# Kernel tuning notes

Hardware: AMD Instinct MI355X
Metric: run time of the kernel (lower is better)

## Reference

```python
import jax, jax.numpy as jnp
import numpy as np
import math

B, N, EMB, DK = 4, 4096, 512, 64

def setup_inputs() -> dict:
    key = jax.random.key(0)
    ks = jax.random.split(key, 4)
    E = jax.random.normal(ks[0], (B, N, EMB), dtype=jnp.float32)
    mask = jnp.tril(jnp.ones((1, N, N), dtype=jnp.int32))  # causal mask, 0 = masked
    s = 1.0 / math.sqrt(EMB)
    wq_kernel = jax.random.normal(ks[1], (EMB, DK), dtype=jnp.float32) * s
    wk_kernel = jax.random.normal(ks[2], (EMB, DK), dtype=jnp.float32) * s
    wv_kernel = jax.random.normal(ks[3], (EMB, EMB), dtype=jnp.float32) * s
    return {
        "E": E, "mask": mask,
        "wq_kernel": wq_kernel, "wq_bias": jnp.zeros((DK,), jnp.float32),
        "wk_kernel": wk_kernel, "wk_bias": jnp.zeros((DK,), jnp.float32),
        "wv_kernel": wv_kernel, "wv_bias": jnp.zeros((EMB,), jnp.float32),
    }

def reference(E, mask, wq_kernel, wq_bias, wk_kernel, wk_bias, wv_kernel, wv_bias):
    # Dense projections (flax Dense: x @ kernel + bias)
    Q = jnp.einsum('bne,ed->bnd', E, wq_kernel) + wq_bias   # [B,N,DK]
    K = jnp.einsum('bne,ed->bnd', E, wk_kernel) + wk_bias   # [B,N,DK]
    V = jnp.einsum('bne,ed->bnd', E, wv_kernel) + wv_bias   # [B,N,EMB]
    scores = jnp.einsum('bqd,bkd->bqk', Q, K) / math.sqrt(Q.shape[-1])  # [B,N,N]
    scores = jnp.where(mask == 0, float('-inf'), scores)
    attention = jax.nn.softmax(scores, axis=-1)
    return jnp.einsum('bqk,bke->bqe', attention, V)  # [B,N,EMB]
```

## Files before the change

kernel.cpp:

```cpp
#include <hip/hip_runtime.h>
#include <hip/hip_bf16.h>

typedef float f32x4 __attribute__((ext_vector_type(4)));
typedef __bf16 bf16x8 __attribute__((ext_vector_type(8)));
typedef __bf16 bf16x4 __attribute__((ext_vector_type(4)));
typedef unsigned short ushort4v __attribute__((ext_vector_type(4)));
typedef unsigned short ushort8v __attribute__((ext_vector_type(8)));

#define MFMA16(a, b, c) __builtin_amdgcn_mfma_f32_16x16x32_bf16((a), (b), (c), 0, 0, 0)

__device__ __forceinline__ unsigned short f2bf(float f) {
    union { float f; unsigned int u; } v; v.f = f;
    unsigned int r = (v.u + 0x7fffu + ((v.u >> 16) & 1u)) >> 16;
    return (unsigned short)r;
}
__device__ __forceinline__ int imin(int a, int b) { return a < b ? a : b; }
__device__ __forceinline__ float fexp2(float x) {
    float r; asm("v_exp_f32 %0, %1" : "=v"(r) : "v"(x)); return r;
}

__device__ __forceinline__ void ldsbar() {
    asm volatile("s_waitcnt lgkmcnt(0)" ::: "memory");
    __builtin_amdgcn_s_barrier();
}

__global__ __launch_bounds__(256) void prep_w(const float* __restrict__ wq,
                                              const float* __restrict__ wk,
                                              const float* __restrict__ wv,
                                              unsigned short* __restrict__ Fqk,
                                              unsigned short* __restrict__ Fv)
{
    const int t = blockIdx.x * 256 + threadIdx.x;
    if (t < 8192) {
        const int lane = t & 63, kt = (t >> 6) & 15, ct = t >> 10;
        const int g = lane >> 4, li = lane & 15;
        const int c = ct * 16 + li;
        const int k0 = kt * 32 + g * 8;
        ushort8v u;
        if (c < 64) {
#pragma unroll
            for (int j = 0; j < 8; ++j) u[j] = f2bf(wq[(size_t)(k0 + j) * 64 + c]);
        } else {
#pragma unroll
            for (int j = 0; j < 8; ++j) u[j] = f2bf(wk[(size_t)(k0 + j) * 64 + (c - 64)]);
        }
        *(ushort8v*)&Fqk[(size_t)t * 8] = u;
    } else {
        const int t2 = t - 8192;
        const int lane = t2 & 63, kt = (t2 >> 6) & 15, ct = t2 >> 10;
        const int g = lane >> 4, li = lane & 15;
        const int c = ct * 16 + li;
        const int k0 = kt * 32 + g * 8;
        ushort8v u;
#pragma unroll
        for (int j = 0; j < 8; ++j) u[j] = f2bf(wv[(size_t)(k0 + j) * 512 + c]);
        *(ushort8v*)&Fv[(size_t)t2 * 8] = u;
    }
}

__global__ __launch_bounds__(512) void proj_kernel(const float* __restrict__ E,
        const unsigned short* __restrict__ Fqk, const unsigned short* __restrict__ Fv,
        const float* __restrict__ bq, const float* __restrict__ bk, const float* __restrict__ bv,
        unsigned short* __restrict__ Qb, unsigned short* __restrict__ Kb,
        unsigned short* __restrict__ Vt)
{
    __shared__ __align__(16) unsigned short Al[2][128][40];

    const int tid = threadIdx.x;
    const int w = tid >> 6, l = tid & 63, g = l >> 4, li = l & 15;
    const int wm = w >> 2, wn = w & 3;
    const int bx = blockIdx.x, by = blockIdx.y;
    const int row0 = bx * 128;
    const int arow = tid >> 2, ak = (tid & 3) * 8;
    const float* ebase = &E[(size_t)(row0 + arow) * 512 + ak];
    const float QSCALE = 0.125f * 1.4426950408889634f;

#define LOAD_E(kt, dst)                                                          \
    {                                                                            \
        const float* ep = ebase + (kt) * 32;                                     \
        f32x4 v0 = *(const f32x4*)ep;                                            \
        f32x4 v1 = *(const f32x4*)(ep + 4);                                      \
        _Pragma("unroll")                                                        \
        for (int j = 0; j < 4; ++j) { dst[j] = f2bf(v0[j]); dst[4 + j] = f2bf(v1[j]); } \
    }

    if (by == 0) {
        f32x4 acc[4][2];
#pragma unroll
        for (int mb = 0; mb < 4; ++mb)
#pragma unroll
            for (int nb = 0; nb < 2; ++nb) acc[mb][nb] = (f32x4)0.0f;

        bf16x8 bw[2], bwn[2];
        {
            ushort8v e0; LOAD_E(0, e0);
            *(ushort8v*)&Al[0][arow][ak] = e0;
#pragma unroll
            for (int nb = 0; nb < 2; ++nb) {
                const int ct = wn * 2 + nb;
                bw[nb] = *(const bf16x8*)&Fqk[((size_t)(ct * 16 + 0) * 64 + l) * 8];
            }
        }
        ldsbar();

        for (int kt = 0; kt < 16; ++kt) {
            const int buf = kt & 1;
            ushort8v en;
            if (kt < 15) LOAD_E(kt + 1, en);
            const int ktn = imin(kt + 1, 15);
#pragma unroll
            for (int nb = 0; nb < 2; ++nb) {
                const int ct = wn * 2 + nb;
                bwn[nb] = *(const bf16x8*)&Fqk[((size_t)(ct * 16 + ktn) * 64 + l) * 8];
            }
            bf16x8 af[4];
#pragma unroll
            for (int mb = 0; mb < 4; ++mb)
                af[mb] = *(const bf16x8*)&Al[buf][wm * 64 + mb * 16 + li][8 * g];
#pragma unroll
            for (int mb = 0; mb < 4; ++mb)
#pragma unroll
                for (int nb = 0; nb < 2; ++nb) acc[mb][nb] = MFMA16(af[mb], bw[nb], acc[mb][nb]);
            if (kt < 15) *(ushort8v*)&Al[buf ^ 1][arow][ak] = en;
            ldsbar();
            bw[0] = bwn[0]; bw[1] = bwn[1];
        }

#pragma unroll
        for (int mb = 0; mb < 4; ++mb) {
#pragma unroll
            for (int nb = 0; nb < 2; ++nb) {
                const int coll = wn * 32 + nb * 16 + li;
                const int grow0 = row0 + wm * 64 + mb * 16 + 4 * g;
                if (coll < 64) {
                    const float bb = bq[coll];
#pragma unroll
                    for (int r = 0; r < 4; ++r)
                        Qb[(size_t)(grow0 + r) * 64 + coll] = f2bf((acc[mb][nb][r] + bb) * QSCALE);
                } else {
                    const float bb = bk[coll - 64];
#pragma unroll
                    for (int r = 0; r < 4; ++r)
                        Kb[(size_t)(grow0 + r) * 64 + (coll - 64)] = f2bf(acc[mb][nb][r] + bb);
                }
            }
        }
    } else {
        const int vy = by - 1;
        f32x4 acc[4][4];
#pragma unroll
        for (int mb = 0; mb < 4; ++mb)
#pragma unroll
            for (int nb = 0; nb < 4; ++nb) acc[mb][nb] = (f32x4)0.0f;

        bf16x8 bw[4], bwn[4];
        {
            ushort8v e0; LOAD_E(0, e0);
            *(ushort8v*)&Al[0][arow][ak] = e0;
#pragma unroll
            for (int nb = 0; nb < 4; ++nb) {
                const int ct = vy * 16 + wn * 4 + nb;
                bw[nb] = *(const bf16x8*)&Fv[((size_t)(ct * 16 + 0) * 64 + l) * 8];
            }
        }
        ldsbar();

        for (int kt = 0; kt < 16; ++kt) {
            const int buf = kt & 1;
            ushort8v en;
            if (kt < 15) LOAD_E(kt + 1, en);
            const int ktn = imin(kt + 1, 15);
#pragma unroll
            for (int nb = 0; nb < 4; ++nb) {
                const int ct = vy * 16 + wn * 4 + nb;
                bwn[nb] = *(const bf16x8*)&Fv[((size_t)(ct * 16 + ktn) * 64 + l) * 8];
            }
            bf16x8 af[4];
#pragma unroll
            for (int mb = 0; mb < 4; ++mb)
                af[mb] = *(const bf16x8*)&Al[buf][wm * 64 + mb * 16 + li][8 * g];
#pragma unroll
            for (int mb = 0; mb < 4; ++mb)
#pragma unroll
                for (int nb = 0; nb < 4; ++nb) acc[mb][nb] = MFMA16(af[mb], bw[nb], acc[mb][nb]);
            if (kt < 15) *(ushort8v*)&Al[buf ^ 1][arow][ak] = en;
            ldsbar();
#pragma unroll
            for (int nb = 0; nb < 4; ++nb) bw[nb] = bwn[nb];
        }

#pragma unroll
        for (int mb = 0; mb < 4; ++mb) {
#pragma unroll
            for (int nb = 0; nb < 4; ++nb) {
                const int col = vy * 256 + wn * 64 + nb * 16 + li;
                const int grow0 = row0 + wm * 64 + mb * 16 + 4 * g;
                const float bb = bv[col];
                ushort4v u;
#pragma unroll
                for (int r = 0; r < 4; ++r) u[r] = f2bf(acc[mb][nb][r] + bb);
                const int bbatch = grow0 >> 12, n = grow0 & 4095;
                *(ushort4v*)(Vt + ((size_t)bbatch * 512 + col) * 4096 + n) = u;
            }
        }
    }
#undef LOAD_E
}

__global__ __launch_bounds__(256) void attn_kernel(const unsigned short* __restrict__ Qb,
                                                   const unsigned short* __restrict__ Kb,
                                                   const unsigned short* __restrict__ Vt,
                                                   float* __restrict__ out)
{
    __shared__ __align__(16) unsigned short Kl[2][64][64];
    __shared__ __align__(16) unsigned short Pl[2][64][76];
    __shared__ float scl[2][64];
    __shared__ __align__(16) float dfl[2][4];
    __shared__ float lsum_l[64];

    const int tid = threadIdx.x;
    const int w = tid >> 6, lane = tid & 63, g = lane >> 4, li = lane & 15;
    const int bid = blockIdx.x;
    const int x = bid >> 4, b = (bid >> 2) & 3, ch = bid & 3;
    const int k4 = x >> 4, r4 = x & 15;
    const int qt = (k4 == 0) ? r4 : (k4 == 1) ? (63 - r4) : (k4 == 2) ? (16 + r4) : (47 - r4);
    const int q0 = qt * 64;
    const int niter = qt + 1;
    const int qrow = 16 * w + li;

    const unsigned short* qptr = Qb + ((size_t)(b * 4096 + q0 + qrow)) * 64 + 8 * g;
    const bf16x8 QA0 = *(const bf16x8*)qptr;
    const bf16x8 QA1 = *(const bf16x8*)(qptr + 32);

    float m_r = -INFINITY, l_r = 0.0f;
    f32x4 Of[4][2];
#pragma unroll
    for (int qb = 0; qb < 4; ++qb) { Of[qb][0] = (f32x4)0.0f; Of[qb][1] = (f32x4)0.0f; }

    const int cglob = ch * 128 + w * 32 + li;
    const unsigned short* vbase = Vt + ((size_t)(b * 512 + cglob)) * 4096 + 8 * g;

    const int krow = tid >> 3, kch = tid & 7;
    const unsigned short* kgb = Kb + ((size_t)(b * 4096 + krow)) * 64 + kch * 8;
    const int kslot = (kch ^ (krow & 7)) * 8;

    {
        ushort8v v0 = *(const ushort8v*)(kgb);
        ushort8v v1 = *(const ushort8v*)(kgb + 32 * 64);
        *(ushort8v*)&Kl[0][krow][kslot] = v0;
        *(ushort8v*)&Kl[0][krow + 32][kslot] = v1;
    }
    ldsbar();

    for (int j = 0; j < niter; ++j) {
        const int buf = j & 1;
        const size_t kv0 = (size_t)j * 64;
        const bool havenext = (j + 1 < niter);

        const size_t kvn = (size_t)imin(j + 1, qt) * 4096;
        ushort8v kn0 = *(const ushort8v*)(kgb + kvn);
        ushort8v kn1 = *(const ushort8v*)(kgb + kvn + 32 * 64);

        bf16x8 VA[2][2];
#pragma unroll
        for (int cf = 0; cf < 2; ++cf)
#pragma unroll
            for (int ks = 0; ks < 2; ++ks)
                VA[cf][ks] = *(const bf16x8*)(vbase + (size_t)cf * 16 * 4096 + kv0 + ks * 32);

        f32x4 S[4];
        {
            const unsigned short(*Kt)[64] = Kl[buf];
            __builtin_amdgcn_s_setprio(1);
#pragma unroll
            for (int cb = 0; cb < 4; ++cb) {
                const int row = cb * 16 + li;
                bf16x8 K0 = *(const bf16x8*)&Kt[row][((g) ^ (row & 7)) * 8];
                bf16x8 K1 = *(const bf16x8*)&Kt[row][((4 + g) ^ (row & 7)) * 8];
                f32x4 s = (f32x4)0.0f;
                s = MFMA16(K0, QA0, s);
                s = MFMA16(K1, QA1, s);
                S[cb] = s;
            }
            __builtin_amdgcn_s_setprio(0);
        }
        if (j == qt) {
#pragma unroll
            for (int cb = 0; cb < 4; ++cb)
#pragma unroll
                for (int rr = 0; rr < 4; ++rr)
                    if (cb * 16 + 4 * g + rr > qrow) S[cb][rr] = -1e30f;
        }
        f32x4 m4 = S[0];
#pragma unroll
        for (int cb = 1; cb < 4; ++cb)
#pragma unroll
            for (int rr = 0; rr < 4; ++rr) m4[rr] = fmaxf(m4[rr], S[cb][rr]);
        const float pmL = fmaxf(fmaxf(m4[0], m4[1]), fmaxf(m4[2], m4[3]));

        const bool nore = __all(pmL - m_r <= 8.0f);
        float sc = 1.0f;
        if (!nore) {
            float pm = fmaxf(pmL, __shfl_xor(pmL, 16));
            pm = fmaxf(pm, __shfl_xor(pm, 32));
            const float mn = fmaxf(m_r, pm);
            sc = fexp2(m_r - mn);
            m_r = mn;
        }
        float rs = 0.0f;
#pragma unroll
        for (int cb = 0; cb < 4; ++cb) {
            bf16x4 pk;
#pragma unroll
            for (int rr = 0; rr < 4; ++rr) {
                const float pv = fexp2(S[cb][rr] - m_r);
                rs += pv;
                pk[rr] = (__bf16)pv;
            }
            *(bf16x4*)&Pl[buf][qrow][cb * 16 + 4 * g] = pk;
        }
        l_r = l_r * sc + rs;
        if (g == 0) scl[buf][qrow] = sc;
        if (lane == 0) dfl[buf][w] = nore ? 1.0f : 0.0f;

        if (havenext) {
            *(ushort8v*)&Kl[buf ^ 1][krow][kslot] = kn0;
            *(ushort8v*)&Kl[buf ^ 1][krow + 32][kslot] = kn1;
        }
        ldsbar();

        f32x4 df = *(const f32x4*)&dfl[buf][0];
        const bool allskip = (df[0] + df[1] + df[2] + df[3]) == 4.0f;
        __builtin_amdgcn_s_setprio(1);
#pragma unroll
        for (int qb = 0; qb < 4; ++qb) {
            bf16x8 PA0 = *(const bf16x8*)&Pl[buf][qb * 16 + li][8 * g];
            bf16x8 PA1 = *(const bf16x8*)&Pl[buf][qb * 16 + li][32 + 8 * g];
            if (!allskip) {
                f32x4 scv = *(const f32x4*)&scl[buf][qb * 16 + 4 * g];
#pragma unroll
                for (int cf = 0; cf < 2; ++cf)
#pragma unroll
                    for (int rr = 0; rr < 4; ++rr) Of[qb][cf][rr] *= scv[rr];
            }
#pragma unroll
            for (int cf = 0; cf < 2; ++cf) {
                f32x4 o = Of[qb][cf];
                o = MFMA16(PA0, VA[cf][0], o);
                o = MFMA16(PA1, VA[cf][1], o);
                Of[qb][cf] = o;
            }
        }
        __builtin_amdgcn_s_setprio(0);
    }

    l_r += __shfl_xor(l_r, 16);
    l_r += __shfl_xor(l_r, 32);
    if (g == 0) lsum_l[qrow] = l_r;
    ldsbar();

    float* obase = out + (size_t)(b * 4096 + q0 + 4 * g) * 512 + cglob;
#pragma unroll
    for (int qb = 0; qb < 4; ++qb) {
        f32x4 lv = *(const f32x4*)&lsum_l[qb * 16 + 4 * g];
#pragma unroll
        for (int cf = 0; cf < 2; ++cf)
#pragma unroll
            for (int rr = 0; rr < 4; ++rr)
                obase[(size_t)(qb * 16 + rr) * 512 + cf * 16] = Of[qb][cf][rr] / lv[rr];
    }
}

extern "C" void kernel_launch(void* const* d_in, const int* in_sizes, int n_in,
                              void* d_out, int out_size, void* d_ws, size_t ws_size,
                              hipStream_t stream)
{
    (void)in_sizes; (void)n_in; (void)out_size; (void)ws_size;
    const float* E  = (const float*)d_in[0];
    const float* wq = (const float*)d_in[2];
    const float* bq = (const float*)d_in[3];
    const float* wk = (const float*)d_in[4];
    const float* bk = (const float*)d_in[5];
    const float* wv = (const float*)d_in[6];
    const float* bv = (const float*)d_in[7];

    const size_t qk_elems = (size_t)4 * 4096 * 64;
    const size_t vt_elems = (size_t)4 * 512 * 4096;

    unsigned short* Qb  = (unsigned short*)d_ws;
    unsigned short* Kb  = Qb + qk_elems;
    unsigned short* Vt  = Kb + qk_elems;
    unsigned short* Fqk = Vt + vt_elems;
    unsigned short* Fv  = Fqk + (size_t)8192 * 8;
    float* out = (float*)d_out;

    prep_w<<<dim3(160), 256, 0, stream>>>(wq, wk, wv, Fqk, Fv);
    proj_kernel<<<dim3(128, 3), 512, 0, stream>>>(E, Fqk, Fv, bq, bk, bv, Qb, Kb, Vt);
    attn_kernel<<<dim3(1024), 256, 0, stream>>>(Qb, Kb, Vt, out);
}
```

Before: 116.0 us.

## Balance causal attention work by splitting heavy query tiles and merging partials

Causal attention work is rebalanced by pairing query tile hi=63-t with lo=t. One block handles the first 33 key tiles of hi. The other handles the remaining key tiles of hi plus all of lo, so every block does roughly 33 iterations. Partial outputs with running max and sum are written to a workspace buffer and combined by a new merge kernel. The aim is to remove the tail imbalance of the triangular workload, at the cost of an extra kernel launch and extra fp32 global traffic for the partials, and only when the workspace is large enough.

```diff
diff --git a/kernel.cpp b/kernel.cpp
--- a/kernel.cpp
+++ b/kernel.cpp
@@ -207,57 +207,30 @@
 #undef LOAD_E
 }
 
-__global__ __launch_bounds__(256) void attn_kernel(const unsigned short* __restrict__ Qb,
-                                                   const unsigned short* __restrict__ Kb,
-                                                   const unsigned short* __restrict__ Vt,
-                                                   float* __restrict__ out)
-{
-    __shared__ __align__(16) unsigned short Kl[2][64][64];
-    __shared__ __align__(16) unsigned short Pl[2][64][76];
-    __shared__ float scl[2][64];
-    __shared__ __align__(16) float dfl[2][4];
-    __shared__ float lsum_l[64];
-
-    const int tid = threadIdx.x;
-    const int w = tid >> 6, lane = tid & 63, g = lane >> 4, li = lane & 15;
-    const int bid = blockIdx.x;
-    const int x = bid >> 4, b = (bid >> 2) & 3, ch = bid & 3;
-    const int k4 = x >> 4, r4 = x & 15;
-    const int qt = (k4 == 0) ? r4 : (k4 == 1) ? (63 - r4) : (k4 == 2) ? (16 + r4) : (47 - r4);
-    const int q0 = qt * 64;
-    const int niter = qt + 1;
-    const int qrow = 16 * w + li;
-
-    const unsigned short* qptr = Qb + ((size_t)(b * 4096 + q0 + qrow)) * 64 + 8 * g;
-    const bf16x8 QA0 = *(const bf16x8*)qptr;
-    const bf16x8 QA1 = *(const bf16x8*)(qptr + 32);
-
-    float m_r = -INFINITY, l_r = 0.0f;
-    f32x4 Of[4][2];
-#pragma unroll
-    for (int qb = 0; qb < 4; ++qb) { Of[qb][0] = (f32x4)0.0f; Of[qb][1] = (f32x4)0.0f; }
-
-    const int cglob = ch * 128 + w * 32 + li;
-    const unsigned short* vbase = Vt + ((size_t)(b * 512 + cglob)) * 4096 + 8 * g;
-
-    const int krow = tid >> 3, kch = tid & 7;
-    const unsigned short* kgb = Kb + ((size_t)(b * 4096 + krow)) * 64 + kch * 8;
-    const int kslot = (kch ^ (krow & 7)) * 8;
-
+__device__ __forceinline__ void attn_segment(int kt0, int cnt, int qcur,
+        const unsigned short* __restrict__ kgb, int krow, int kslot,
+        const unsigned short* __restrict__ vbase,
+        bf16x8 QA0, bf16x8 QA1,
+        int w, int lane, int g, int li, int qrow,
+        float& m_r, float& l_r, f32x4 (&Of)[4][2],
+        unsigned short (*Kl)[64][64], unsigned short (*Pl)[64][76],
+        float (*scl)[64], float (*dfl)[4])
+{
     {
-        ushort8v v0 = *(const ushort8v*)(kgb);
-        ushort8v v1 = *(const ushort8v*)(kgb + 32 * 64);
+        ushort8v v0 = *(const ushort8v*)(kgb + (size_t)kt0 * 4096);
+        ushort8v v1 = *(const ushort8v*)(kgb + (size_t)kt0 * 4096 + 32 * 64);
         *(ushort8v*)&Kl[0][krow][kslot] = v0;
         *(ushort8v*)&Kl[0][krow + 32][kslot] = v1;
     }
     ldsbar();
 
-    for (int j = 0; j < niter; ++j) {
+    for (int j = 0; j < cnt; ++j) {
         const int buf = j & 1;
-        const size_t kv0 = (size_t)j * 64;
-        const bool havenext = (j + 1 < niter);
-
-        const size_t kvn = (size_t)imin(j + 1, qt) * 4096;
+        const int kt = kt0 + j;
+        const size_t kv0 = (size_t)kt * 64;
+        const bool havenext = (j + 1 < cnt);
+
+        const size_t kvn = (size_t)(kt0 + imin(j + 1, cnt - 1)) * 4096;
         ushort8v kn0 = *(const ushort8v*)(kgb + kvn);
         ushort8v kn1 = *(const ushort8v*)(kgb + kvn + 32 * 64);
 
@@ -284,7 +257,7 @@
             }
             __builtin_amdgcn_s_setprio(0);
         }
-        if (j == qt) {
+        if (kt == qcur) {
 #pragma unroll
             for (int cb = 0; cb < 4; ++cb)
 #pragma unroll
@@ -353,6 +326,163 @@
         }
         __builtin_amdgcn_s_setprio(0);
     }
+}
+
+__global__ __launch_bounds__(256) void attn_split(const unsigned short* __restrict__ Qb,
+                                                  const unsigned short* __restrict__ Kb,
+                                                  const unsigned short* __restrict__ Vt,
+                                                  float* __restrict__ Pa,
+                                                  float* __restrict__ out)
+{
+    __shared__ __align__(16) unsigned short Kl[2][64][64];
+    __shared__ __align__(16) unsigned short Pl[2][64][76];
+    __shared__ float scl[2][64];
+    __shared__ __align__(16) float dfl[2][4];
+    __shared__ float lsum_l[64];
+
+    const int tid = threadIdx.x;
+    const int w = tid >> 6, lane = tid & 63, g = lane >> 4, li = lane & 15;
+    const int bid = blockIdx.x;
+    const int half = bid & 1;
+    const int rest = bid >> 1;
+    const int t = rest >> 4, b = (rest >> 2) & 3, ch = rest & 3;
+    const int hi = 63 - t, lo = t;
+    const int qrow = 16 * w + li;
+
+    const int cglob = ch * 128 + w * 32 + li;
+    const unsigned short* vbase = Vt + ((size_t)(b * 512 + cglob)) * 4096 + 8 * g;
+    const int krow = tid >> 3, kch = tid & 7;
+    const unsigned short* kgb = Kb + ((size_t)(b * 4096 + krow)) * 64 + kch * 8;
+    const int kslot = (kch ^ (krow & 7)) * 8;
+
+    float m_r = -INFINITY, l_r = 0.0f;
+    f32x4 Of[4][2];
+#pragma unroll
+    for (int qb = 0; qb < 4; ++qb) { Of[qb][0] = (f32x4)0.0f; Of[qb][1] = (f32x4)0.0f; }
+
+    float* rec = Pa + ((size_t)(half * 512 + rest)) * 8320;
+
+    if (half == 0) {
+        const unsigned short* qptr = Qb + ((size_t)(b * 4096 + hi * 64 + qrow)) * 64 + 8 * g;
+        attn_segment(0, 33, hi, kgb, krow, kslot, vbase,
+                     *(const bf16x8*)qptr, *(const bf16x8*)(qptr + 32),
+                     w, lane, g, li, qrow, m_r, l_r, Of, Kl, Pl, scl, dfl);
+        float lred = l_r + __shfl_xor(l_r, 16);
+        lred += __shfl_xor(lred, 32);
+#pragma unroll
+        for (int qb = 0; qb < 4; ++qb)
+#pragma unroll
+            for (int cf = 0; cf < 2; ++cf)
+#pragma unroll
+                for (int rr = 0; rr < 4; ++rr)
+                    rec[(size_t)(qb * 16 + 4 * g + rr) * 128 + (w * 32 + li) + cf * 16] = Of[qb][cf][rr];
+        if (g == 0) { rec[8192 + qrow] = m_r; rec[8256 + qrow] = lred; }
+    } else {
+        const int cnt1 = 31 - t;
+        if (cnt1 > 0) {
+            const unsigned short* qptr = Qb + ((size_t)(b * 4096 + hi * 64 + qrow)) * 64 + 8 * g;
+            attn_segment(33, cnt1, hi, kgb, krow, kslot, vbase,
+                         *(const bf16x8*)qptr, *(const bf16x8*)(qptr + 32),
+                         w, lane, g, li, qrow, m_r, l_r, Of, Kl, Pl, scl, dfl);
+        }
+        float lred = l_r + __shfl_xor(l_r, 16);
+        lred += __shfl_xor(lred, 32);
+#pragma unroll
+        for (int qb = 0; qb < 4; ++qb)
+#pragma unroll
+            for (int cf = 0; cf < 2; ++cf)
+#pragma unroll
+                for (int rr = 0; rr < 4; ++rr)
+                    rec[(size_t)(qb * 16 + 4 * g + rr) * 128 + (w * 32 + li) + cf * 16] = Of[qb][cf][rr];
+        if (g == 0) { rec[8192 + qrow] = m_r; rec[8256 + qrow] = lred; }
+        m_r = -INFINITY; l_r = 0.0f;
+#pragma unroll
+        for (int qb = 0; qb < 4; ++qb) { Of[qb][0] = (f32x4)0.0f; Of[qb][1] = (f32x4)0.0f; }
+        {
+            const unsigned short* qptr = Qb + ((size_t)(b * 4096 + lo * 64 + qrow)) * 64 + 8 * g;
+            attn_segment(0, t + 1, lo, kgb, krow, kslot, vbase,
+                         *(const bf16x8*)qptr, *(const bf16x8*)(qptr + 32),
+                         w, lane, g, li, qrow, m_r, l_r, Of, Kl, Pl, scl, dfl);
+        }
+        l_r += __shfl_xor(l_r, 16);
+        l_r += __shfl_xor(l_r, 32);
+        if (g == 0) lsum_l[qrow] = l_r;
+        ldsbar();
+        float* obase = out + (size_t)(b * 4096 + lo * 64 + 4 * g) * 512 + cglob;
+#pragma unroll
+        for (int qb = 0; qb < 4; ++qb) {
+            f32x4 lv = *(const f32x4*)&lsum_l[qb * 16 + 4 * g];
+#pragma unroll
+            for (int cf = 0; cf < 2; ++cf)
+#pragma unroll
+                for (int rr = 0; rr < 4; ++rr)
+                    obase[(size_t)(qb * 16 + rr) * 512 + cf * 16] = Of[qb][cf][rr] / lv[rr];
+        }
+    }
+}
+
+__global__ __launch_bounds__(256) void merge_kernel(const float* __restrict__ Pa,
+                                                    float* __restrict__ out)
+{
+    const int pid = blockIdx.x;
+    const int t = pid >> 4, b = (pid >> 2) & 3, ch = pid & 3;
+    const int hi = 63 - t;
+    const float* A = Pa + (size_t)pid * 8320;
+    const float* B = Pa + (size_t)(512 + pid) * 8320;
+    const int tid = threadIdx.x;
+#pragma unroll
+    for (int k = 0; k < 8; ++k) {
+        const int vidx = k * 256 + tid;
+        const int row = vidx >> 5;
+        const int col4 = (vidx & 31) * 4;
+        const float ma = A[8192 + row], mb = B[8192 + row];
+        const float mF = fmaxf(ma, mb);
+        const float aA = fexp2(ma - mF), aB = fexp2(mb - mF);
+        const float l = aA * A[8256 + row] + aB * B[8256 + row];
+        f32x4 oa = *(const f32x4*)&A[(size_t)row * 128 + col4];
+        f32x4 ob = *(const f32x4*)&B[(size_t)row * 128 + col4];
+        f32x4 r;
+#pragma unroll
+        for (int j = 0; j < 4; ++j) r[j] = (aA * oa[j] + aB * ob[j]) / l;
+        *(f32x4*)&out[((size_t)(b * 4096 + hi * 64 + row)) * 512 + ch * 128 + col4] = r;
+    }
+}
+
+__global__ __launch_bounds__(256) void attn_kernel(const unsigned short* __restrict__ Qb,
+                                                   const unsigned short* __restrict__ Kb,
+                                                   const unsigned short* __restrict__ Vt,
+                                                   float* __restrict__ out)
+{
+    __shared__ __align__(16) unsigned short Kl[2][64][64];
+    __shared__ __align__(16) unsigned short Pl[2][64][76];
+    __shared__ float scl[2][64];
+    __shared__ __align__(16) float dfl[2][4];
+    __shared__ float lsum_l[64];
+
+    const int tid = threadIdx.x;
+    const int w = tid >> 6, lane = tid & 63, g = lane >> 4, li = lane & 15;
+    const int bid = blockIdx.x;
+    const int x = bid >> 4, b = (bid >> 2) & 3, ch = bid & 3;
+    const int k4 = x >> 4, r4 = x & 15;
+    const int qt = (k4 == 0) ? r4 : (k4 == 1) ? (63 - r4) : (k4 == 2) ? (16 + r4) : (47 - r4);
+    const int q0 = qt * 64;
+    const int qrow = 16 * w + li;
+
+    const int cglob = ch * 128 + w * 32 + li;
+    const unsigned short* vbase = Vt + ((size_t)(b * 512 + cglob)) * 4096 + 8 * g;
+    const int krow = tid >> 3, kch = tid & 7;
+    const unsigned short* kgb = Kb + ((size_t)(b * 4096 + krow)) * 64 + kch * 8;
+    const int kslot = (kch ^ (krow & 7)) * 8;
+
+    float m_r = -INFINITY, l_r = 0.0f;
+    f32x4 Of[4][2];
+#pragma unroll
+    for (int qb = 0; qb < 4; ++qb) { Of[qb][0] = (f32x4)0.0f; Of[qb][1] = (f32x4)0.0f; }
+
+    const unsigned short* qptr = Qb + ((size_t)(b * 4096 + q0 + qrow)) * 64 + 8 * g;
+    attn_segment(0, qt + 1, qt, kgb, krow, kslot, vbase,
+                 *(const bf16x8*)qptr, *(const bf16x8*)(qptr + 32),
+                 w, lane, g, li, qrow, m_r, l_r, Of, Kl, Pl, scl, dfl);
 
     l_r += __shfl_xor(l_r, 16);
     l_r += __shfl_xor(l_r, 32);
@@ -375,7 +505,7 @@
                               void* d_out, int out_size, void* d_ws, size_t ws_size,
                               hipStream_t stream)
 {
-    (void)in_sizes; (void)n_in; (void)out_size; (void)ws_size;
+    (void)in_sizes; (void)n_in; (void)out_size;
     const float* E  = (const float*)d_in[0];
     const float* wq = (const float*)d_in[2];
     const float* bq = (const float*)d_in[3];
@@ -392,9 +522,18 @@
     unsigned short* Vt  = Kb + qk_elems;
     unsigned short* Fqk = Vt + vt_elems;
     unsigned short* Fv  = Fqk + (size_t)8192 * 8;
+    float* Pa = (float*)(Fv + (size_t)32768 * 8);
     float* out = (float*)d_out;
+
+    const size_t base_bytes = (2 * qk_elems + vt_elems + (size_t)8192 * 8 + (size_t)32768 * 8) * 2;
+    const size_t need_split = base_bytes + (size_t)1024 * 8320 * 4;
 
     prep_w<<<dim3(160), 256, 0, stream>>>(wq, wk, wv, Fqk, Fv);
     proj_kernel<<<dim3(128, 3), 512, 0, stream>>>(E, Fqk, Fv, bq, bk, bv, Qb, Kb, Vt);
-    attn_kernel<<<dim3(1024), 256, 0, stream>>>(Qb, Kb, Vt, out);
-}
+    if (ws_size >= need_split) {
+        attn_split<<<dim3(1024), 256, 0, stream>>>(Qb, Kb, Vt, Pa, out);
+        merge_kernel<<<dim3(512), 256, 0, stream>>>(Pa, out);
+    } else {
+        attn_kernel<<<dim3(1024), 256, 0, stream>>>(Qb, Kb, Vt, out);
+    }
+}
```

Measured after the change: 208.4 us. 79.6% more time.

## Shrink attention query tile to 32 rows with 2 waves per block

Applied to the files above, without the earlier changes.

The attention kernel now processes 32 query rows per block with 2 waves of 128 threads, each wave covering 64 value columns instead of 32. The grid doubles to 2048 blocks and is scheduled longest-first (reverse query order) instead of the interleaved balancing pattern. The causal mask now uses global positions because a 32-row tile sits inside a 64-key tile. The intent is better load balance and occupancy in the causal workload. The cost is that each key/value tile is reused across fewer query rows, so global loads of K and V per unit of work increase.

```diff
diff --git a/kernel.cpp b/kernel.cpp
--- a/kernel.cpp
+++ b/kernel.cpp
@@ -207,37 +207,39 @@
 #undef LOAD_E
 }
 
-__global__ __launch_bounds__(256) void attn_kernel(const unsigned short* __restrict__ Qb,
+__global__ __launch_bounds__(128) void attn_kernel(const unsigned short* __restrict__ Qb,
                                                    const unsigned short* __restrict__ Kb,
                                                    const unsigned short* __restrict__ Vt,
                                                    float* __restrict__ out)
 {
     __shared__ __align__(16) unsigned short Kl[2][64][64];
-    __shared__ __align__(16) unsigned short Pl[2][64][76];
-    __shared__ float scl[2][64];
-    __shared__ __align__(16) float dfl[2][4];
-    __shared__ float lsum_l[64];
+    __shared__ __align__(16) unsigned short Pl[2][32][76];
+    __shared__ float scl[2][32];
+    __shared__ float dfl[2][2];
+    __shared__ float lsum_l[32];
 
     const int tid = threadIdx.x;
     const int w = tid >> 6, lane = tid & 63, g = lane >> 4, li = lane & 15;
     const int bid = blockIdx.x;
     const int x = bid >> 4, b = (bid >> 2) & 3, ch = bid & 3;
-    const int k4 = x >> 4, r4 = x & 15;
-    const int qt = (k4 == 0) ? r4 : (k4 == 1) ? (63 - r4) : (k4 == 2) ? (16 + r4) : (47 - r4);
-    const int q0 = qt * 64;
-    const int niter = qt + 1;
+    const int qi = 127 - x;
+    const int q0 = qi * 32;
+    const int niter = (qi >> 1) + 1;
     const int qrow = 16 * w + li;
-
-    const unsigned short* qptr = Qb + ((size_t)(b * 4096 + q0 + qrow)) * 64 + 8 * g;
+    const int qglob = q0 + qrow;
+
+    const unsigned short* qptr = Qb + ((size_t)(b * 4096 + qglob)) * 64 + 8 * g;
     const bf16x8 QA0 = *(const bf16x8*)qptr;
     const bf16x8 QA1 = *(const bf16x8*)(qptr + 32);
 
     float m_r = -INFINITY, l_r = 0.0f;
-    f32x4 Of[4][2];
-#pragma unroll
-    for (int qb = 0; qb < 4; ++qb) { Of[qb][0] = (f32x4)0.0f; Of[qb][1] = (f32x4)0.0f; }
-
-    const int cglob = ch * 128 + w * 32 + li;
+    f32x4 Of[2][4];
+#pragma unroll
+    for (int qb = 0; qb < 2; ++qb)
+#pragma unroll
+        for (int cf = 0; cf < 4; ++cf) Of[qb][cf] = (f32x4)0.0f;
+
+    const int cglob = ch * 128 + w * 64 + li;
     const unsigned short* vbase = Vt + ((size_t)(b * 512 + cglob)) * 4096 + 8 * g;
 
     const int krow = tid >> 3, kch = tid & 7;
@@ -245,10 +247,11 @@
     const int kslot = (kch ^ (krow & 7)) * 8;
 
     {
-        ushort8v v0 = *(const ushort8v*)(kgb);
-        ushort8v v1 = *(const ushort8v*)(kgb + 32 * 64);
-        *(ushort8v*)&Kl[0][krow][kslot] = v0;
-        *(ushort8v*)&Kl[0][krow + 32][kslot] = v1;
+#pragma unroll
+        for (int i = 0; i < 4; ++i) {
+            ushort8v v = *(const ushort8v*)(kgb + (size_t)(16 * i) * 64);
+            *(ushort8v*)&Kl[0][krow + 16 * i][kslot] = v;
+        }
     }
     ldsbar();
 
@@ -257,13 +260,15 @@
         const size_t kv0 = (size_t)j * 64;
         const bool havenext = (j + 1 < niter);
 
-        const size_t kvn = (size_t)imin(j + 1, qt) * 4096;
-        ushort8v kn0 = *(const ushort8v*)(kgb + kvn);
-        ushort8v kn1 = *(const ushort8v*)(kgb + kvn + 32 * 64);
-
-        bf16x8 VA[2][2];
-#pragma unroll
-        for (int cf = 0; cf < 2; ++cf)
+        const size_t kvn = (size_t)imin(j + 1, niter - 1) * 4096;
+        ushort8v kn[4];
+#pragma unroll
+        for (int i = 0; i < 4; ++i)
+            kn[i] = *(const ushort8v*)(kgb + kvn + (size_t)(16 * i) * 64);
+
+        bf16x8 VA[4][2];
+#pragma unroll
+        for (int cf = 0; cf < 4; ++cf)
 #pragma unroll
             for (int ks = 0; ks < 2; ++ks)
                 VA[cf][ks] = *(const bf16x8*)(vbase + (size_t)cf * 16 * 4096 + kv0 + ks * 32);
@@ -284,12 +289,12 @@
             }
             __builtin_amdgcn_s_setprio(0);
         }
-        if (j == qt) {
+        if (j == niter - 1) {
 #pragma unroll
             for (int cb = 0; cb < 4; ++cb)
 #pragma unroll
                 for (int rr = 0; rr < 4; ++rr)
-                    if (cb * 16 + 4 * g + rr > qrow) S[cb][rr] = -1e30f;
+                    if ((int)kv0 + cb * 16 + 4 * g + rr > qglob) S[cb][rr] = -1e30f;
         }
         f32x4 m4 = S[0];
 #pragma unroll
@@ -324,27 +329,27 @@
         if (lane == 0) dfl[buf][w] = nore ? 1.0f : 0.0f;
 
         if (havenext) {
-            *(ushort8v*)&Kl[buf ^ 1][krow][kslot] = kn0;
-            *(ushort8v*)&Kl[buf ^ 1][krow + 32][kslot] = kn1;
+#pragma unroll
+            for (int i = 0; i < 4; ++i)
+                *(ushort8v*)&Kl[buf ^ 1][krow + 16 * i][kslot] = kn[i];
         }
         ldsbar();
 
-        f32x4 df = *(const f32x4*)&dfl[buf][0];
-        const bool allskip = (df[0] + df[1] + df[2] + df[3]) == 4.0f;
+        const bool allskip = (dfl[buf][0] + dfl[buf][1]) == 2.0f;
         __builtin_amdgcn_s_setprio(1);
 #pragma unroll
-        for (int qb = 0; qb < 4; ++qb) {
+        for (int qb = 0; qb < 2; ++qb) {
             bf16x8 PA0 = *(const bf16x8*)&Pl[buf][qb * 16 + li][8 * g];
             bf16x8 PA1 = *(const bf16x8*)&Pl[buf][qb * 16 + li][32 + 8 * g];
             if (!allskip) {
                 f32x4 scv = *(const f32x4*)&scl[buf][qb * 16 + 4 * g];
 #pragma unroll
-                for (int cf = 0; cf < 2; ++cf)
+                for (int cf = 0; cf < 4; ++cf)
 #pragma unroll
                     for (int rr = 0; rr < 4; ++rr) Of[qb][cf][rr] *= scv[rr];
             }
 #pragma unroll
-            for (int cf = 0; cf < 2; ++cf) {
+            for (int cf = 0; cf < 4; ++cf) {
                 f32x4 o = Of[qb][cf];
                 o = MFMA16(PA0, VA[cf][0], o);
                 o = MFMA16(PA1, VA[cf][1], o);
@@ -361,10 +366,10 @@
 
     float* obase = out + (size_t)(b * 4096 + q0 + 4 * g) * 512 + cglob;
 #pragma unroll
-    for (int qb = 0; qb < 4; ++qb) {
+    for (int qb = 0; qb < 2; ++qb) {
         f32x4 lv = *(const f32x4*)&lsum_l[qb * 16 + 4 * g];
 #pragma unroll
-        for (int cf = 0; cf < 2; ++cf)
+        for (int cf = 0; cf < 4; ++cf)
 #pragma unroll
             for (int rr = 0; rr < 4; ++rr)
                 obase[(size_t)(qb * 16 + rr) * 512 + cf * 16] = Of[qb][cf][rr] / lv[rr];
@@ -396,5 +401,5 @@
 
     prep_w<<<dim3(160), 256, 0, stream>>>(wq, wk, wv, Fqk, Fv);
     proj_kernel<<<dim3(128, 3), 512, 0, stream>>>(E, Fqk, Fv, bq, bk, bv, Qb, Kb, Vt);
-    attn_kernel<<<dim3(1024), 256, 0, stream>>>(Qb, Kb, Vt, out);
-}
+    attn_kernel<<<dim3(2048), 128, 0, stream>>>(Qb, Kb, Vt, out);
+}
```

Result: slower. 180.5 us (+55.5%).
